# Optimization experiments

Hardware: AMD Instinct MI355X
Metric: run time of the kernel (lower is better)

Reference implementation:

```python
import jax, jax.numpy as jnp
import numpy as np

DIM = 192
HEADS = 6
WS = 8                      # window size (Wh = Ww = 8)
N = WS * WS                 # tokens per window = 64
NW = 1024                   # windows per image (256/8)^2
BATCH = 2
B_ = NW * BATCH             # 2048 windows total
TABLE = (2 * WS - 1) ** 2   # 225 relative-position entries


def _relative_position_index():
    coords = np.stack(np.meshgrid(np.arange(WS), np.arange(WS), indexing='ij'))  # (2,WS,WS)
    cf = coords.reshape(2, -1)                       # (2, N)
    rc = (cf[:, :, None] - cf[:, None, :]).transpose(1, 2, 0).astype(np.int64)  # (N,N,2)
    rc[..., 0] += WS - 1
    rc[..., 1] += WS - 1
    rc[..., 0] *= 2 * WS - 1
    return rc.sum(-1)                                # (N, N) in [0, TABLE)


def setup_inputs() -> dict:
    key = jax.random.key(0)
    ks = jax.random.split(key, 16)
    s = 0.02
    inp = {
        'x': jax.random.normal(ks[0], (B_, N, DIM), jnp.float32),
        'y': jax.random.normal(ks[1], (B_, N, DIM), jnp.float32),
        'mask_x': jnp.zeros((NW, N, N), jnp.float32),
        'mask_y': jnp.zeros((NW, N, N), jnp.float32),
        'qkv_w': jax.random.normal(ks[2], (3 * DIM, DIM), jnp.float32) * s,
        'qkv_b': jnp.zeros((3 * DIM,), jnp.float32),
        'kv_w': jax.random.normal(ks[3], (2 * DIM, DIM), jnp.float32) * s,
        'kv_b': jnp.zeros((2 * DIM,), jnp.float32),
        'rpb_x': jax.random.normal(ks[4], (TABLE, HEADS), jnp.float32) * s,
        'rpb_y': jax.random.normal(ks[5], (TABLE, HEADS), jnp.float32) * s,
        'merge1_w': jax.random.normal(ks[6], (DIM, 2 * DIM), jnp.float32) * s,
        'merge1_b': jnp.zeros((DIM,), jnp.float32),
        'merge2_w': jax.random.normal(ks[7], (DIM, DIM), jnp.float32) * s,
        'merge2_b': jnp.zeros((DIM,), jnp.float32),
        'proj_w': jax.random.normal(ks[8], (DIM, DIM), jnp.float32) * s,
        'proj_b': jnp.zeros((DIM,), jnp.float32),
        'rel_idx': jnp.asarray(_relative_position_index(), jnp.int32),
    }
    return inp


def _attend(q, k, v, table, rel_idx, mask):
    # q,k,v: (B_, H, N, hd); table: (TABLE, H); mask: (nW, N, N)
    b_, h, n, hd = q.shape
    bias = table[rel_idx].transpose(2, 0, 1)                 # (H, N, N)
    attn = jnp.einsum('bhnd,bhmd->bhnm', q, k) + bias[None]  # (B_, H, N, N)
    nW = mask.shape[0]
    attn = attn.reshape(b_ // nW, nW, h, n, n) + mask[None, :, None]
    attn = jax.nn.softmax(attn.reshape(b_, h, n, n), axis=-1)
    out = jnp.einsum('bhnm,bhmd->bhnd', attn, v)             # (B_, H, N, hd)
    return out.transpose(0, 2, 1, 3).reshape(b_, n, h * hd)


def reference(x, y, mask_x, mask_y, qkv_w, qkv_b, kv_w, kv_b, rpb_x, rpb_y,
              merge1_w, merge1_b, merge2_w, merge2_b, proj_w, proj_b, rel_idx):
    b_, n, c = x.shape
    hd = c // HEADS
    scale = hd ** (-0.5)
    qkv = (x @ qkv_w.T + qkv_b).reshape(b_, n, 3, HEADS, hd).transpose(2, 0, 3, 1, 4)
    q, k, v = qkv[0] * scale, qkv[1], qkv[2]
    x_self = _attend(q, k, v, rpb_x, rel_idx, mask_x)
    kv = (y @ kv_w.T + kv_b).reshape(b_, n, 2, HEADS, hd).transpose(2, 0, 3, 1, 4)
    x_cross = _attend(q, kv[0], kv[1], rpb_y, rel_idx, mask_y)
    m = jnp.concatenate([x_self, x_cross], axis=-1) @ merge1_w.T + merge1_b
    m = jax.nn.leaky_relu(m, negative_slope=0.2)
    m = m @ merge2_w.T + merge2_b
    return m @ proj_w.T + proj_b
```

## Files before the change

### kernel.cpp

```cpp
#include <hip/hip_runtime.h>

#define DEVINL __device__ __forceinline__

typedef __attribute__((ext_vector_type(8))) short          s16x8;
typedef __attribute__((ext_vector_type(8))) unsigned short u16x8;
typedef __attribute__((ext_vector_type(4))) unsigned short u16x4;
typedef __attribute__((ext_vector_type(4))) float          f32x4;

DEVINL unsigned short f2b(float f) {
    union { float f; unsigned int u; } c; c.f = f;
    return (unsigned short)((c.u + 0x7FFFu + ((c.u >> 16) & 1u)) >> 16);
}
DEVINL f32x4 mfma16(s16x8 a, s16x8 b, f32x4 c) {
    return __builtin_amdgcn_mfma_f32_16x16x32_bf16(a, b, c, 0, 0, 0);
}

#define QKV_ELEMS 110592
#define KV_ELEMS  73728
#define M1_ELEMS  73728
#define M2_ELEMS  36864
#define PW_ELEMS  36864
#define O_QKV 0
#define O_KV  110592
#define O_M1  184320
#define O_M2  258048
#define O_PW  294912
#define WB_ELEMS 331776
#define WB_BYTES (WB_ELEMS * 2)

#define LD_IN  200
#define LD_K   200
#define LD_VT  72
#define LD_P   72
#define LD_CAT 392
#define LD_M   200
#define OFF_R1 0
#define OFF_R2 12800
#define OFF_R3 25600
#define SMEM_ELEMS 39424
#define CATB OFF_R2

#define SCALE 0.17677669529663687f
#define LOG2E 1.4426950408889634f

__global__ __launch_bounds__(256) void cvt_w(
    const float* __restrict__ a, const float* __restrict__ b, const float* __restrict__ c,
    const float* __restrict__ d, const float* __restrict__ e, unsigned short* __restrict__ o)
{
    int i = (blockIdx.x * 256 + threadIdx.x) * 4;
    if (i >= WB_ELEMS) return;
    const float* s; int off;
    if (i < O_KV)      { s = a; off = i - O_QKV; }
    else if (i < O_M1) { s = b; off = i - O_KV; }
    else if (i < O_M2) { s = c; off = i - O_M1; }
    else if (i < O_PW) { s = d; off = i - O_M2; }
    else               { s = e; off = i - O_PW; }
    float4 v = *(const float4*)(s + off);
    u16x4 r;
    r[0] = f2b(v.x); r[1] = f2b(v.y); r[2] = f2b(v.z); r[3] = f2b(v.w);
    *(u16x4*)(o + i) = r;
}

template<bool WB>
DEVINL s16x8 loadB(const unsigned short* wbp, const float* wfp, int off) {
    if constexpr (WB) {
        return *(const s16x8*)(wbp + off);
    } else {
        float4 v0 = *(const float4*)(wfp + off);
        float4 v1 = *(const float4*)(wfp + off + 4);
        s16x8 r;
        r[0] = (short)f2b(v0.x); r[1] = (short)f2b(v0.y); r[2] = (short)f2b(v0.z); r[3] = (short)f2b(v0.w);
        r[4] = (short)f2b(v1.x); r[5] = (short)f2b(v1.y); r[6] = (short)f2b(v1.z); r[7] = (short)f2b(v1.w);
        return r;
    }
}

template<bool WB>
__global__ __launch_bounds__(512, 4) void swin_fused(
    const float* __restrict__ x,
    const float* __restrict__ y,
    const float* __restrict__ mask_x,
    const float* __restrict__ mask_y,
    const float* __restrict__ qkv_w,
    const float* __restrict__ qkv_b,
    const float* __restrict__ kv_w,
    const float* __restrict__ kv_b,
    const float* __restrict__ rpb_x,
    const float* __restrict__ rpb_y,
    const float* __restrict__ m1w,
    const float* __restrict__ m1b,
    const float* __restrict__ m2w,
    const float* __restrict__ m2b,
    const float* __restrict__ pw,
    const float* __restrict__ pb,
    const int* __restrict__ rel_idx,
    const unsigned short* __restrict__ wb,
    float* __restrict__ out)
{
    __shared__ __align__(16) unsigned short smem[SMEM_ELEMS];

    const int tid  = threadIdx.x;
    const int w    = tid >> 6;
    const int lane = tid & 63;
    const int l16  = lane & 15;
    const int quad = lane >> 4;
    const int wm   = w >> 2;
    const int wn   = w & 3;
    const int rb   = w >> 1;
    const int hh   = w & 1;
    const int b    = blockIdx.x;
    const int widx = b & 1023;

    const unsigned short* wqkv = WB ? wb + O_QKV : nullptr;
    const unsigned short* wkv  = WB ? wb + O_KV  : nullptr;
    const unsigned short* wm1  = WB ? wb + O_M1  : nullptr;
    const unsigned short* wm2  = WB ? wb + O_M2  : nullptr;
    const unsigned short* wpw  = WB ? wb + O_PW  : nullptr;

    {
        const float4* gx = (const float4*)(x + (size_t)b * 64 * 192);
        #pragma unroll
        for (int it = 0; it < 3; ++it) {
            int c = it * 512 + tid;
            int e = c * 8;
            int row = e / 192, col = e - row * 192;
            float4 v0 = gx[c * 2], v1 = gx[c * 2 + 1];
            u16x8 r;
            r[0] = f2b(v0.x); r[1] = f2b(v0.y); r[2] = f2b(v0.z); r[3] = f2b(v0.w);
            r[4] = f2b(v1.x); r[5] = f2b(v1.y); r[6] = f2b(v1.z); r[7] = f2b(v1.w);
            *(u16x8*)&smem[OFF_R1 + row * LD_IN + col] = r;
        }
    }
    __syncthreads();

    {
        s16x8 afr[2][6];
        #pragma unroll
        for (int mt = 0; mt < 2; ++mt)
            #pragma unroll
            for (int ks = 0; ks < 6; ++ks)
                afr[mt][ks] = *(const s16x8*)&smem[OFF_R1 + (wm * 32 + mt * 16 + l16) * LD_IN + ks * 32 + quad * 8];
        __syncthreads();

        #pragma unroll
        for (int nt = 0; nt < 9; ++nt) {
            int n0  = wn * 144 + nt * 16;
            int col = n0 + l16;
            f32x4 acc0 = {0,0,0,0}, acc1 = {0,0,0,0};
            #pragma unroll
            for (int ks = 0; ks < 6; ++ks) {
                s16x8 bf = loadB<WB>(wqkv, qkv_w, col * 192 + ks * 32 + quad * 8);
                acc0 = mfma16(afr[0][ks], bf, acc0);
                acc1 = mfma16(afr[1][ks], bf, acc1);
            }
            f32x4 accv[2] = {acc0, acc1};
            float bias = qkv_b[col];
            if (n0 < 192) {
                #pragma unroll
                for (int mt = 0; mt < 2; ++mt)
                    #pragma unroll
                    for (int r = 0; r < 4; ++r)
                        smem[OFF_R1 + (wm * 32 + mt * 16 + quad * 4 + r) * LD_K + col] =
                            f2b((accv[mt][r] + bias) * SCALE);
            } else if (n0 < 384) {
                #pragma unroll
                for (int mt = 0; mt < 2; ++mt)
                    #pragma unroll
                    for (int r = 0; r < 4; ++r)
                        smem[OFF_R2 + (wm * 32 + mt * 16 + quad * 4 + r) * LD_K + (col - 192)] =
                            f2b(accv[mt][r] + bias);
            } else {
                #pragma unroll
                for (int mt = 0; mt < 2; ++mt)
                    #pragma unroll
                    for (int r = 0; r < 4; ++r)
                        smem[OFF_R3 + (col - 384) * LD_VT + (wm * 32 + mt * 16 + quad * 4 + r)] =
                            f2b(accv[mt][r] + bias);
            }
        }
    }
    __syncthreads();

    s16x8 aQ[3];
    #pragma unroll
    for (int hl = 0; hl < 3; ++hl)
        aQ[hl] = *(const s16x8*)&smem[OFF_R1 + (rb * 16 + l16) * LD_K + (hh * 3 + hl) * 32 + quad * 8];
    __syncthreads();

    auto do_attn = [&](const float* __restrict__ rpb,
                       const float* __restrict__ mask,
                       unsigned (&opk)[12]) {
        unsigned idxp[8];
        #pragma unroll
        for (int p = 0; p < 8; ++p) {
            int ntt = p >> 1, r0 = (p & 1) * 2;
            int row = rb * 16 + quad * 4;
            int col = ntt * 16 + l16;
            unsigned lo = (unsigned)rel_idx[(row + r0)     * 64 + col] * 6u;
            unsigned hi = (unsigned)rel_idx[(row + r0 + 1) * 64 + col] * 6u;
            idxp[p] = lo | (hi << 16);
        }
        const float* mrow = mask + (size_t)widx * 4096 + (rb * 16 + quad * 4) * 64 + l16;
        const int pbase = OFF_R1 + w * 16 * LD_P;
        #pragma unroll
        for (int hl = 0; hl < 3; ++hl) {
            int h = hh * 3 + hl;
            f32x4 sacc[4];
            #pragma unroll
            for (int ntt = 0; ntt < 4; ++ntt) {
                s16x8 bK = *(const s16x8*)&smem[OFF_R2 + (ntt * 16 + l16) * LD_K + h * 32 + quad * 8];
                f32x4 z = {0,0,0,0};
                sacc[ntt] = mfma16(aQ[hl], bK, z);
            }
            float sv[4][4];
            #pragma unroll
            for (int ntt = 0; ntt < 4; ++ntt)
                #pragma unroll
                for (int r = 0; r < 4; ++r) {
                    unsigned idx6 = (idxp[ntt * 2 + (r >> 1)] >> ((r & 1) * 16)) & 0xFFFFu;
                    sv[ntt][r] = sacc[ntt][r] + rpb[idx6 + h] + mrow[r * 64 + ntt * 16];
                }
            float pv[4][4];
            #pragma unroll
            for (int r = 0; r < 4; ++r) {
                float mx = fmaxf(fmaxf(sv[0][r], sv[1][r]), fmaxf(sv[2][r], sv[3][r]));
                mx = fmaxf(mx, __shfl_xor(mx, 1));
                mx = fmaxf(mx, __shfl_xor(mx, 2));
                mx = fmaxf(mx, __shfl_xor(mx, 4));
                mx = fmaxf(mx, __shfl_xor(mx, 8));
                float e0 = __builtin_amdgcn_exp2f((sv[0][r] - mx) * LOG2E);
                float e1 = __builtin_amdgcn_exp2f((sv[1][r] - mx) * LOG2E);
                float e2 = __builtin_amdgcn_exp2f((sv[2][r] - mx) * LOG2E);
                float e3 = __builtin_amdgcn_exp2f((sv[3][r] - mx) * LOG2E);
                float s = e0 + e1 + e2 + e3;
                s += __shfl_xor(s, 1);
                s += __shfl_xor(s, 2);
                s += __shfl_xor(s, 4);
                s += __shfl_xor(s, 8);
                float inv = __builtin_amdgcn_rcpf(s);
                pv[0][r] = e0 * inv; pv[1][r] = e1 * inv; pv[2][r] = e2 * inv; pv[3][r] = e3 * inv;
            }
            #pragma unroll
            for (int ntt = 0; ntt < 4; ++ntt)
                #pragma unroll
                for (int r = 0; r < 4; ++r)
                    smem[pbase + (quad * 4 + r) * LD_P + ntt * 16 + l16] = f2b(pv[ntt][r]);
            f32x4 oh0 = {0,0,0,0}, oh1 = {0,0,0,0};
            #pragma unroll
            for (int kt = 0; kt < 2; ++kt) {
                s16x8 aP  = *(const s16x8*)&smem[pbase + l16 * LD_P + kt * 32 + quad * 8];
                s16x8 bV0 = *(const s16x8*)&smem[OFF_R3 + (h * 32 + l16) * LD_VT + kt * 32 + quad * 8];
                s16x8 bV1 = *(const s16x8*)&smem[OFF_R3 + (h * 32 + 16 + l16) * LD_VT + kt * 32 + quad * 8];
                oh0 = mfma16(aP, bV0, oh0);
                oh1 = mfma16(aP, bV1, oh1);
            }
            #pragma unroll
            for (int r = 0; r < 4; ++r)
                opk[hl * 4 + r] = (unsigned)f2b(oh0[r]) | ((unsigned)f2b(oh1[r]) << 16);
        }
    };

    unsigned opks[12];
    do_attn(rpb_x, mask_x, opks);
    __syncthreads();

    {
        const float4* gy = (const float4*)(y + (size_t)b * 64 * 192);
        #pragma unroll
        for (int it = 0; it < 3; ++it) {
            int c = it * 512 + tid;
            int e = c * 8;
            int row = e / 192, col = e - row * 192;
            float4 v0 = gy[c * 2], v1 = gy[c * 2 + 1];
            u16x8 r;
            r[0] = f2b(v0.x); r[1] = f2b(v0.y); r[2] = f2b(v0.z); r[3] = f2b(v0.w);
            r[4] = f2b(v1.x); r[5] = f2b(v1.y); r[6] = f2b(v1.z); r[7] = f2b(v1.w);
            *(u16x8*)&smem[OFF_R1 + row * LD_IN + col] = r;
        }
    }
    __syncthreads();

    {
        s16x8 afr[2][6];
        #pragma unroll
        for (int mt = 0; mt < 2; ++mt)
            #pragma unroll
            for (int ks = 0; ks < 6; ++ks)
                afr[mt][ks] = *(const s16x8*)&smem[OFF_R1 + (wm * 32 + mt * 16 + l16) * LD_IN + ks * 32 + quad * 8];

        #pragma unroll
        for (int nt = 0; nt < 6; ++nt) {
            int n0  = wn * 96 + nt * 16;
            int col = n0 + l16;
            f32x4 acc0 = {0,0,0,0}, acc1 = {0,0,0,0};
            #pragma unroll
            for (int ks = 0; ks < 6; ++ks) {
                s16x8 bf = loadB<WB>(wkv, kv_w, col * 192 + ks * 32 + quad * 8);
                acc0 = mfma16(afr[0][ks], bf, acc0);
                acc1 = mfma16(afr[1][ks], bf, acc1);
            }
            f32x4 accv[2] = {acc0, acc1};
            float bias = kv_b[col];
            if (n0 < 192) {
                #pragma unroll
                for (int mt = 0; mt < 2; ++mt)
                    #pragma unroll
                    for (int r = 0; r < 4; ++r)
                        smem[OFF_R2 + (wm * 32 + mt * 16 + quad * 4 + r) * LD_K + col] =
                            f2b(accv[mt][r] + bias);
            } else {
                #pragma unroll
                for (int mt = 0; mt < 2; ++mt)
                    #pragma unroll
                    for (int r = 0; r < 4; ++r)
                        smem[OFF_R3 + (col - 192) * LD_VT + (wm * 32 + mt * 16 + quad * 4 + r)] =
                            f2b(accv[mt][r] + bias);
            }
        }
    }
    __syncthreads();

    unsigned opkc[12];
    do_attn(rpb_y, mask_y, opkc);
    __syncthreads();

    #pragma unroll
    for (int hl = 0; hl < 3; ++hl) {
        int h = hh * 3 + hl;
        #pragma unroll
        for (int r = 0; r < 4; ++r) {
            int row = rb * 16 + quad * 4 + r;
            unsigned ps = opks[hl * 4 + r];
            unsigned pc = opkc[hl * 4 + r];
            smem[CATB + row * LD_CAT + h * 32 + l16]             = (unsigned short)(ps & 0xFFFFu);
            smem[CATB + row * LD_CAT + h * 32 + 16 + l16]        = (unsigned short)(ps >> 16);
            smem[CATB + row * LD_CAT + 192 + h * 32 + l16]       = (unsigned short)(pc & 0xFFFFu);
            smem[CATB + row * LD_CAT + 192 + h * 32 + 16 + l16]  = (unsigned short)(pc >> 16);
        }
    }
    __syncthreads();

    {
        f32x4 acc[3][2];
        #pragma unroll
        for (int nt = 0; nt < 3; ++nt) { f32x4 z = {0,0,0,0}; acc[nt][0] = z; acc[nt][1] = z; }
        #pragma unroll
        for (int ks = 0; ks < 12; ++ks) {
            s16x8 c0 = *(const s16x8*)&smem[CATB + (wm * 32 + l16) * LD_CAT + ks * 32 + quad * 8];
            s16x8 c1 = *(const s16x8*)&smem[CATB + (wm * 32 + 16 + l16) * LD_CAT + ks * 32 + quad * 8];
            #pragma unroll
            for (int nt = 0; nt < 3; ++nt) {
                int col = wn * 48 + nt * 16 + l16;
                s16x8 bf = loadB<WB>(wm1, m1w, col * 384 + ks * 32 + quad * 8);
                acc[nt][0] = mfma16(c0, bf, acc[nt][0]);
                acc[nt][1] = mfma16(c1, bf, acc[nt][1]);
            }
        }
        #pragma unroll
        for (int nt = 0; nt < 3; ++nt) {
            int col = wn * 48 + nt * 16 + l16;
            float bias = m1b[col];
            #pragma unroll
            for (int mt = 0; mt < 2; ++mt)
                #pragma unroll
                for (int r = 0; r < 4; ++r) {
                    float v = acc[nt][mt][r] + bias;
                    v = (v > 0.f) ? v : 0.2f * v;
                    smem[OFF_R1 + (wm * 32 + mt * 16 + quad * 4 + r) * LD_M + col] = f2b(v);
                }
        }
    }
    __syncthreads();

    {
        s16x8 afr[2][6];
        #pragma unroll
        for (int mt = 0; mt < 2; ++mt)
            #pragma unroll
            for (int ks = 0; ks < 6; ++ks)
                afr[mt][ks] = *(const s16x8*)&smem[OFF_R1 + (wm * 32 + mt * 16 + l16) * LD_M + ks * 32 + quad * 8];

        #pragma unroll
        for (int nt = 0; nt < 3; ++nt) {
            int n0  = wn * 48 + nt * 16;
            int col = n0 + l16;
            f32x4 acc0 = {0,0,0,0}, acc1 = {0,0,0,0};
            #pragma unroll
            for (int ks = 0; ks < 6; ++ks) {
                s16x8 bf = loadB<WB>(wm2, m2w, col * 192 + ks * 32 + quad * 8);
                acc0 = mfma16(afr[0][ks], bf, acc0);
                acc1 = mfma16(afr[1][ks], bf, acc1);
            }
            f32x4 accv[2] = {acc0, acc1};
            float bias = m2b[col];
            #pragma unroll
            for (int mt = 0; mt < 2; ++mt)
                #pragma unroll
                for (int r = 0; r < 4; ++r)
                    smem[OFF_R2 + (wm * 32 + mt * 16 + quad * 4 + r) * LD_M + col] = f2b(accv[mt][r] + bias);
        }
    }
    __syncthreads();

    {
        s16x8 afr[2][6];
        #pragma unroll
        for (int mt = 0; mt < 2; ++mt)
            #pragma unroll
            for (int ks = 0; ks < 6; ++ks)
                afr[mt][ks] = *(const s16x8*)&smem[OFF_R2 + (wm * 32 + mt * 16 + l16) * LD_M + ks * 32 + quad * 8];

        #pragma unroll
        for (int nt = 0; nt < 3; ++nt) {
            int n0  = wn * 48 + nt * 16;
            int col = n0 + l16;
            f32x4 acc0 = {0,0,0,0}, acc1 = {0,0,0,0};
            #pragma unroll
            for (int ks = 0; ks < 6; ++ks) {
                s16x8 bf = loadB<WB>(wpw, pw, col * 192 + ks * 32 + quad * 8);
                acc0 = mfma16(afr[0][ks], bf, acc0);
                acc1 = mfma16(afr[1][ks], bf, acc1);
            }
            f32x4 accv[2] = {acc0, acc1};
            float bias = pb[col];
            #pragma unroll
            for (int mt = 0; mt < 2; ++mt)
                #pragma unroll
                for (int r = 0; r < 4; ++r) {
                    int row = wm * 32 + mt * 16 + quad * 4 + r;
                    out[((size_t)b * 64 + row) * 192 + col] = accv[mt][r] + bias;
                }
        }
    }
}

extern "C" void kernel_launch(void* const* d_in, const int* in_sizes, int n_in,
                              void* d_out, int out_size, void* d_ws, size_t ws_size,
                              hipStream_t stream) {
    (void)in_sizes; (void)n_in; (void)out_size;
    const float* x    = (const float*)d_in[0];
    const float* y    = (const float*)d_in[1];
    const float* mx   = (const float*)d_in[2];
    const float* my   = (const float*)d_in[3];
    const float* qw   = (const float*)d_in[4];
    const float* qb   = (const float*)d_in[5];
    const float* kw   = (const float*)d_in[6];
    const float* kb   = (const float*)d_in[7];
    const float* rx   = (const float*)d_in[8];
    const float* ry   = (const float*)d_in[9];
    const float* m1w  = (const float*)d_in[10];
    const float* m1b  = (const float*)d_in[11];
    const float* m2w  = (const float*)d_in[12];
    const float* m2b  = (const float*)d_in[13];
    const float* pw   = (const float*)d_in[14];
    const float* pb   = (const float*)d_in[15];
    const int*   ridx = (const int*)d_in[16];
    float* out = (float*)d_out;

    if (ws_size >= (size_t)WB_BYTES) {
        unsigned short* wbuf = (unsigned short*)d_ws;
        cvt_w<<<WB_ELEMS / 4 / 256, 256, 0, stream>>>(qw, kw, m1w, m2w, pw, wbuf);
        swin_fused<true><<<2048, 512, 0, stream>>>(
            x, y, mx, my, qw, qb, kw, kb, rx, ry, m1w, m1b, m2w, m2b, pw, pb, ridx,
            wbuf, out);
    } else {
        swin_fused<false><<<2048, 512, 0, stream>>>(
            x, y, mx, my, qw, qb, kw, kb, rx, ry, m1w, m1b, m2w, m2b, pw, pb, ridx,
            nullptr, out);
    }
}
```

Measured before the change: 652.3 us.

## Process two windows per block to double weight reuse per B-fragment load

Each block now handles two 64-token windows (128 rows), so every weight fragment loaded from global memory feeds four MFMA row tiles instead of two. The grid halves to 1024 blocks, shared memory roughly doubles to about 154KB, and each warp does full six-head attention for one row block of one window. The aim is to halve weight traffic per token. The cost is more registers (launch bounds drop to two blocks per CU), lower occupancy, and fewer blocks to spread across CUs.

Result: faster. 523.9 us (-19.7%).

```diff
diff --git a/kernel.cpp b/kernel.cpp
--- a/kernel.cpp
+++ b/kernel.cpp
@@ -35,9 +35,10 @@
 #define LD_CAT 392
 #define LD_M   200
 #define OFF_R1 0
-#define OFF_R2 12800
-#define OFF_R3 25600
-#define SMEM_ELEMS 39424
+#define OFF_R2 25600
+#define OFF_R3 51200
+#define VT_WIN 13824
+#define SMEM_ELEMS 78848
 #define CATB OFF_R2
 
 #define SCALE 0.17677669529663687f
@@ -76,7 +77,7 @@
 }
 
 template<bool WB>
-__global__ __launch_bounds__(512, 4) void swin_fused(
+__global__ __launch_bounds__(512, 2) void swin_fused(
     const float* __restrict__ x,
     const float* __restrict__ y,
     const float* __restrict__ mask_x,
@@ -104,12 +105,11 @@
     const int lane = tid & 63;
     const int l16  = lane & 15;
     const int quad = lane >> 4;
+    const int wn   = w & 3;
     const int wm   = w >> 2;
-    const int wn   = w & 3;
-    const int rb   = w >> 1;
-    const int hh   = w & 1;
+    const int win  = w >> 2;
+    const int rb   = w & 3;
     const int b    = blockIdx.x;
-    const int widx = b & 1023;
 
     const unsigned short* wqkv = WB ? wb + O_QKV : nullptr;
     const unsigned short* wkv  = WB ? wb + O_KV  : nullptr;
@@ -118,9 +118,9 @@
     const unsigned short* wpw  = WB ? wb + O_PW  : nullptr;
 
     {
-        const float4* gx = (const float4*)(x + (size_t)b * 64 * 192);
-        #pragma unroll
-        for (int it = 0; it < 3; ++it) {
+        const float4* gx = (const float4*)(x + (size_t)b * 128 * 192);
+        #pragma unroll
+        for (int it = 0; it < 6; ++it) {
             int c = it * 512 + tid;
             int e = c * 8;
             int row = e / 192, col = e - row * 192;
@@ -134,62 +134,65 @@
     __syncthreads();
 
     {
-        s16x8 afr[2][6];
-        #pragma unroll
-        for (int mt = 0; mt < 2; ++mt)
+        s16x8 afr[4][6];
+        #pragma unroll
+        for (int mt = 0; mt < 4; ++mt)
             #pragma unroll
             for (int ks = 0; ks < 6; ++ks)
-                afr[mt][ks] = *(const s16x8*)&smem[OFF_R1 + (wm * 32 + mt * 16 + l16) * LD_IN + ks * 32 + quad * 8];
+                afr[mt][ks] = *(const s16x8*)&smem[OFF_R1 + (wm * 64 + mt * 16 + l16) * LD_IN + ks * 32 + quad * 8];
         __syncthreads();
 
         #pragma unroll
         for (int nt = 0; nt < 9; ++nt) {
             int n0  = wn * 144 + nt * 16;
             int col = n0 + l16;
-            f32x4 acc0 = {0,0,0,0}, acc1 = {0,0,0,0};
+            f32x4 a0 = {0,0,0,0}, a1 = {0,0,0,0}, a2 = {0,0,0,0}, a3 = {0,0,0,0};
             #pragma unroll
             for (int ks = 0; ks < 6; ++ks) {
                 s16x8 bf = loadB<WB>(wqkv, qkv_w, col * 192 + ks * 32 + quad * 8);
-                acc0 = mfma16(afr[0][ks], bf, acc0);
-                acc1 = mfma16(afr[1][ks], bf, acc1);
-            }
-            f32x4 accv[2] = {acc0, acc1};
+                a0 = mfma16(afr[0][ks], bf, a0);
+                a1 = mfma16(afr[1][ks], bf, a1);
+                a2 = mfma16(afr[2][ks], bf, a2);
+                a3 = mfma16(afr[3][ks], bf, a3);
+            }
+            f32x4 accv[4] = {a0, a1, a2, a3};
             float bias = qkv_b[col];
             if (n0 < 192) {
                 #pragma unroll
-                for (int mt = 0; mt < 2; ++mt)
+                for (int mt = 0; mt < 4; ++mt)
                     #pragma unroll
                     for (int r = 0; r < 4; ++r)
-                        smem[OFF_R1 + (wm * 32 + mt * 16 + quad * 4 + r) * LD_K + col] =
+                        smem[OFF_R1 + (wm * 64 + mt * 16 + quad * 4 + r) * LD_K + col] =
                             f2b((accv[mt][r] + bias) * SCALE);
             } else if (n0 < 384) {
                 #pragma unroll
-                for (int mt = 0; mt < 2; ++mt)
+                for (int mt = 0; mt < 4; ++mt)
                     #pragma unroll
                     for (int r = 0; r < 4; ++r)
-                        smem[OFF_R2 + (wm * 32 + mt * 16 + quad * 4 + r) * LD_K + (col - 192)] =
+                        smem[OFF_R2 + (wm * 64 + mt * 16 + quad * 4 + r) * LD_K + (col - 192)] =
                             f2b(accv[mt][r] + bias);
             } else {
                 #pragma unroll
-                for (int mt = 0; mt < 2; ++mt)
+                for (int mt = 0; mt < 4; ++mt)
                     #pragma unroll
                     for (int r = 0; r < 4; ++r)
-                        smem[OFF_R3 + (col - 384) * LD_VT + (wm * 32 + mt * 16 + quad * 4 + r)] =
+                        smem[OFF_R3 + wm * VT_WIN + (col - 384) * LD_VT + (mt * 16 + quad * 4 + r)] =
                             f2b(accv[mt][r] + bias);
             }
         }
     }
     __syncthreads();
 
-    s16x8 aQ[3];
+    s16x8 aQ[6];
     #pragma unroll
-    for (int hl = 0; hl < 3; ++hl)
-        aQ[hl] = *(const s16x8*)&smem[OFF_R1 + (rb * 16 + l16) * LD_K + (hh * 3 + hl) * 32 + quad * 8];
+    for (int h = 0; h < 6; ++h)
+        aQ[h] = *(const s16x8*)&smem[OFF_R1 + (win * 64 + rb * 16 + l16) * LD_K + h * 32 + quad * 8];
     __syncthreads();
 
     auto do_attn = [&](const float* __restrict__ rpb,
                        const float* __restrict__ mask,
-                       unsigned (&opk)[12]) {
+                       unsigned (&opk)[24]) {
+        int widx = (b * 2 + win) & 1023;
         unsigned idxp[8];
         #pragma unroll
         for (int p = 0; p < 8; ++p) {
@@ -203,14 +206,13 @@
         const float* mrow = mask + (size_t)widx * 4096 + (rb * 16 + quad * 4) * 64 + l16;
         const int pbase = OFF_R1 + w * 16 * LD_P;
         #pragma unroll
-        for (int hl = 0; hl < 3; ++hl) {
-            int h = hh * 3 + hl;
+        for (int h = 0; h < 6; ++h) {
             f32x4 sacc[4];
             #pragma unroll
             for (int ntt = 0; ntt < 4; ++ntt) {
-                s16x8 bK = *(const s16x8*)&smem[OFF_R2 + (ntt * 16 + l16) * LD_K + h * 32 + quad * 8];
+                s16x8 bK = *(const s16x8*)&smem[OFF_R2 + (win * 64 + ntt * 16 + l16) * LD_K + h * 32 + quad * 8];
                 f32x4 z = {0,0,0,0};
-                sacc[ntt] = mfma16(aQ[hl], bK, z);
+                sacc[ntt] = mfma16(aQ[h], bK, z);
             }
             float sv[4][4];
             #pragma unroll
@@ -249,25 +251,25 @@
             #pragma unroll
             for (int kt = 0; kt < 2; ++kt) {
                 s16x8 aP  = *(const s16x8*)&smem[pbase + l16 * LD_P + kt * 32 + quad * 8];
-                s16x8 bV0 = *(const s16x8*)&smem[OFF_R3 + (h * 32 + l16) * LD_VT + kt * 32 + quad * 8];
-                s16x8 bV1 = *(const s16x8*)&smem[OFF_R3 + (h * 32 + 16 + l16) * LD_VT + kt * 32 + quad * 8];
+                s16x8 bV0 = *(const s16x8*)&smem[OFF_R3 + win * VT_WIN + (h * 32 + l16) * LD_VT + kt * 32 + quad * 8];
+                s16x8 bV1 = *(const s16x8*)&smem[OFF_R3 + win * VT_WIN + (h * 32 + 16 + l16) * LD_VT + kt * 32 + quad * 8];
                 oh0 = mfma16(aP, bV0, oh0);
                 oh1 = mfma16(aP, bV1, oh1);
             }
             #pragma unroll
             for (int r = 0; r < 4; ++r)
-                opk[hl * 4 + r] = (unsigned)f2b(oh0[r]) | ((unsigned)f2b(oh1[r]) << 16);
+                opk[h * 4 + r] = (unsigned)f2b(oh0[r]) | ((unsigned)f2b(oh1[r]) << 16);
         }
     };
 
-    unsigned opks[12];
+    unsigned opks[24];
     do_attn(rpb_x, mask_x, opks);
     __syncthreads();
 
     {
-        const float4* gy = (const float4*)(y + (size_t)b * 64 * 192);
-        #pragma unroll
-        for (int it = 0; it < 3; ++it) {
+        const float4* gy = (const float4*)(y + (size_t)b * 128 * 192);
+        #pragma unroll
+        for (int it = 0; it < 6; ++it) {
             int c = it * 512 + tid;
             int e = c * 8;
             int row = e / 192, col = e - row * 192;
@@ -281,57 +283,58 @@
     __syncthreads();
 
     {
-        s16x8 afr[2][6];
-        #pragma unroll
-        for (int mt = 0; mt < 2; ++mt)
+        s16x8 afr[4][6];
+        #pragma unroll
+        for (int mt = 0; mt < 4; ++mt)
             #pragma unroll
             for (int ks = 0; ks < 6; ++ks)
-                afr[mt][ks] = *(const s16x8*)&smem[OFF_R1 + (wm * 32 + mt * 16 + l16) * LD_IN + ks * 32 + quad * 8];
+                afr[mt][ks] = *(const s16x8*)&smem[OFF_R1 + (wm * 64 + mt * 16 + l16) * LD_IN + ks * 32 + quad * 8];
 
         #pragma unroll
         for (int nt = 0; nt < 6; ++nt) {
             int n0  = wn * 96 + nt * 16;
             int col = n0 + l16;
-            f32x4 acc0 = {0,0,0,0}, acc1 = {0,0,0,0};
+            f32x4 a0 = {0,0,0,0}, a1 = {0,0,0,0}, a2 = {0,0,0,0}, a3 = {0,0,0,0};
             #pragma unroll
             for (int ks = 0; ks < 6; ++ks) {
                 s16x8 bf = loadB<WB>(wkv, kv_w, col * 192 + ks * 32 + quad * 8);
-                acc0 = mfma16(afr[0][ks], bf, acc0);
-                acc1 = mfma16(afr[1][ks], bf, acc1);
-            }
-            f32x4 accv[2] = {acc0, acc1};
+                a0 = mfma16(afr[0][ks], bf, a0);
+                a1 = mfma16(afr[1][ks], bf, a1);
+                a2 = mfma16(afr[2][ks], bf, a2);
+                a3 = mfma16(afr[3][ks], bf, a3);
+            }
+            f32x4 accv[4] = {a0, a1, a2, a3};
             float bias = kv_b[col];
             if (n0 < 192) {
                 #pragma unroll
-                for (int mt = 0; mt < 2; ++mt)
+                for (int mt = 0; mt < 4; ++mt)
                     #pragma unroll
                     for (int r = 0; r < 4; ++r)
-                        smem[OFF_R2 + (wm * 32 + mt * 16 + quad * 4 + r) * LD_K + col] =
+                        smem[OFF_R2 + (wm * 64 + mt * 16 + quad * 4 + r) * LD_K + col] =
                             f2b(accv[mt][r] + bias);
             } else {
                 #pragma unroll
-                for (int mt = 0; mt < 2; ++mt)
+                for (int mt = 0; mt < 4; ++mt)
                     #pragma unroll
                     for (int r = 0; r < 4; ++r)
-                        smem[OFF_R3 + (col - 192) * LD_VT + (wm * 32 + mt * 16 + quad * 4 + r)] =
+                        smem[OFF_R3 + wm * VT_WIN + (col - 192) * LD_VT + (mt * 16 + quad * 4 + r)] =
                             f2b(accv[mt][r] + bias);
             }
         }
     }
     __syncthreads();
 
-    unsigned opkc[12];
+    unsigned opkc[24];
     do_attn(rpb_y, mask_y, opkc);
     __syncthreads();
 
     #pragma unroll
-    for (int hl = 0; hl < 3; ++hl) {
-        int h = hh * 3 + hl;
+    for (int h = 0; h < 6; ++h) {
         #pragma unroll
         for (int r = 0; r < 4; ++r) {
-            int row = rb * 16 + quad * 4 + r;
-            unsigned ps = opks[hl * 4 + r];
-            unsigned pc = opkc[hl * 4 + r];
+            int row = win * 64 + rb * 16 + quad * 4 + r;
+            unsigned ps = opks[h * 4 + r];
+            unsigned pc = opkc[h * 4 + r];
             smem[CATB + row * LD_CAT + h * 32 + l16]             = (unsigned short)(ps & 0xFFFFu);
             smem[CATB + row * LD_CAT + h * 32 + 16 + l16]        = (unsigned short)(ps >> 16);
             smem[CATB + row * LD_CAT + 192 + h * 32 + l16]       = (unsigned short)(pc & 0xFFFFu);
@@ -341,19 +344,24 @@
     __syncthreads();
 
     {
-        f32x4 acc[3][2];
-        #pragma unroll
-        for (int nt = 0; nt < 3; ++nt) { f32x4 z = {0,0,0,0}; acc[nt][0] = z; acc[nt][1] = z; }
+        f32x4 acc[3][4];
+        #pragma unroll
+        for (int nt = 0; nt < 3; ++nt)
+            #pragma unroll
+            for (int mt = 0; mt < 4; ++mt) { f32x4 z = {0,0,0,0}; acc[nt][mt] = z; }
         #pragma unroll
         for (int ks = 0; ks < 12; ++ks) {
-            s16x8 c0 = *(const s16x8*)&smem[CATB + (wm * 32 + l16) * LD_CAT + ks * 32 + quad * 8];
-            s16x8 c1 = *(const s16x8*)&smem[CATB + (wm * 32 + 16 + l16) * LD_CAT + ks * 32 + quad * 8];
+            s16x8 cm[4];
+            #pragma unroll
+            for (int mt = 0; mt < 4; ++mt)
+                cm[mt] = *(const s16x8*)&smem[CATB + (wm * 64 + mt * 16 + l16) * LD_CAT + ks * 32 + quad * 8];
             #pragma unroll
             for (int nt = 0; nt < 3; ++nt) {
                 int col = wn * 48 + nt * 16 + l16;
                 s16x8 bf = loadB<WB>(wm1, m1w, col * 384 + ks * 32 + quad * 8);
-                acc[nt][0] = mfma16(c0, bf, acc[nt][0]);
-                acc[nt][1] = mfma16(c1, bf, acc[nt][1]);
+                #pragma unroll
+                for (int mt = 0; mt < 4; ++mt)
+                    acc[nt][mt] = mfma16(cm[mt], bf, acc[nt][mt]);
             }
         }
         #pragma unroll
@@ -361,74 +369,76 @@
             int col = wn * 48 + nt * 16 + l16;
             float bias = m1b[col];
             #pragma unroll
-            for (int mt = 0; mt < 2; ++mt)
+            for (int mt = 0; mt < 4; ++mt)
                 #pragma unroll
                 for (int r = 0; r < 4; ++r) {
                     float v = acc[nt][mt][r] + bias;
                     v = (v > 0.f) ? v : 0.2f * v;
-                    smem[OFF_R1 + (wm * 32 + mt * 16 + quad * 4 + r) * LD_M + col] = f2b(v);
+                    smem[OFF_R1 + (wm * 64 + mt * 16 + quad * 4 + r) * LD_M + col] = f2b(v);
                 }
         }
     }
     __syncthreads();
 
     {
-        s16x8 afr[2][6];
-        #pragma unroll
-        for (int mt = 0; mt < 2; ++mt)
+        s16x8 afr[4][6];
+        #pragma unroll
+        for (int mt = 0; mt < 4; ++mt)
             #pragma unroll
             for (int ks = 0; ks < 6; ++ks)
-                afr[mt][ks] = *(const s16x8*)&smem[OFF_R1 + (wm * 32 + mt * 16 + l16) * LD_M + ks * 32 + quad * 8];
+                afr[mt][ks] = *(const s16x8*)&smem[OFF_R1 + (wm * 64 + mt * 16 + l16) * LD_M + ks * 32 + quad * 8];
 
         #pragma unroll
         for (int nt = 0; nt < 3; ++nt) {
-            int n0  = wn * 48 + nt * 16;
-            int col = n0 + l16;
-            f32x4 acc0 = {0,0,0,0}, acc1 = {0,0,0,0};
+            int col = wn * 48 + nt * 16 + l16;
+            f32x4 a0 = {0,0,0,0}, a1 = {0,0,0,0}, a2 = {0,0,0,0}, a3 = {0,0,0,0};
             #pragma unroll
             for (int ks = 0; ks < 6; ++ks) {
                 s16x8 bf = loadB<WB>(wm2, m2w, col * 192 + ks * 32 + quad * 8);
-                acc0 = mfma16(afr[0][ks], bf, acc0);
-                acc1 = mfma16(afr[1][ks], bf, acc1);
-            }
-            f32x4 accv[2] = {acc0, acc1};
+                a0 = mfma16(afr[0][ks], bf, a0);
+                a1 = mfma16(afr[1][ks], bf, a1);
+                a2 = mfma16(afr[2][ks], bf, a2);
+                a3 = mfma16(afr[3][ks], bf, a3);
+            }
+            f32x4 accv[4] = {a0, a1, a2, a3};
             float bias = m2b[col];
             #pragma unroll
-            for (int mt = 0; mt < 2; ++mt)
+            for (int mt = 0; mt < 4; ++mt)
                 #pragma unroll
                 for (int r = 0; r < 4; ++r)
-                    smem[OFF_R2 + (wm * 32 + mt * 16 + quad * 4 + r) * LD_M + col] = f2b(accv[mt][r] + bias);
-        }
-    }
-    __syncthreads();
-
-    {
-        s16x8 afr[2][6];
-        #pragma unroll
-        for (int mt = 0; mt < 2; ++mt)
+                    smem[OFF_R2 + (wm * 64 + mt * 16 + quad * 4 + r) * LD_M + col] = f2b(accv[mt][r] + bias);
+        }
+    }
+    __syncthreads();
+
+    {
+        s16x8 afr[4][6];
+        #pragma unroll
+        for (int mt = 0; mt < 4; ++mt)
             #pragma unroll
             for (int ks = 0; ks < 6; ++ks)
-                afr[mt][ks] = *(const s16x8*)&smem[OFF_R2 + (wm * 32 + mt * 16 + l16) * LD_M + ks * 32 + quad * 8];
+                afr[mt][ks] = *(const s16x8*)&smem[OFF_R2 + (wm * 64 + mt * 16 + l16) * LD_M + ks * 32 + quad * 8];
 
         #pragma unroll
         for (int nt = 0; nt < 3; ++nt) {
-            int n0  = wn * 48 + nt * 16;
-            int col = n0 + l16;
-            f32x4 acc0 = {0,0,0,0}, acc1 = {0,0,0,0};
+            int col = wn * 48 + nt * 16 + l16;
+            f32x4 a0 = {0,0,0,0}, a1 = {0,0,0,0}, a2 = {0,0,0,0}, a3 = {0,0,0,0};
             #pragma unroll
             for (int ks = 0; ks < 6; ++ks) {
                 s16x8 bf = loadB<WB>(wpw, pw, col * 192 + ks * 32 + quad * 8);
-                acc0 = mfma16(afr[0][ks], bf, acc0);
-                acc1 = mfma16(afr[1][ks], bf, acc1);
-            }
-            f32x4 accv[2] = {acc0, acc1};
+                a0 = mfma16(afr[0][ks], bf, a0);
+                a1 = mfma16(afr[1][ks], bf, a1);
+                a2 = mfma16(afr[2][ks], bf, a2);
+                a3 = mfma16(afr[3][ks], bf, a3);
+            }
+            f32x4 accv[4] = {a0, a1, a2, a3};
             float bias = pb[col];
             #pragma unroll
-            for (int mt = 0; mt < 2; ++mt)
+            for (int mt = 0; mt < 4; ++mt)
                 #pragma unroll
                 for (int r = 0; r < 4; ++r) {
-                    int row = wm * 32 + mt * 16 + quad * 4 + r;
-                    out[((size_t)b * 64 + row) * 192 + col] = accv[mt][r] + bias;
+                    int row = wm * 64 + mt * 16 + quad * 4 + r;
+                    out[((size_t)b * 128 + row) * 192 + col] = accv[mt][r] + bias;
                 }
         }
     }
@@ -460,11 +470,11 @@
     if (ws_size >= (size_t)WB_BYTES) {
         unsigned short* wbuf = (unsigned short*)d_ws;
         cvt_w<<<WB_ELEMS / 4 / 256, 256, 0, stream>>>(qw, kw, m1w, m2w, pw, wbuf);
-        swin_fused<true><<<2048, 512, 0, stream>>>(
+        swin_fused<true><<<1024, 512, 0, stream>>>(
             x, y, mx, my, qw, qb, kw, kb, rx, ry, m1w, m1b, m2w, m2b, pw, pb, ridx,
             wbuf, out);
     } else {
-        swin_fused<false><<<2048, 512, 0, stream>>>(
+        swin_fused<false><<<1024, 512, 0, stream>>>(
             x, y, mx, my, qw, qb, kw, kb, rx, ry, m1w, m1b, m2w, m2b, pw, pb, ridx,
             nullptr, out);
     }
```

## Process two windows per block with 1024 threads and doubled shared memory

Applied to the files above, without the earlier changes.

Each block now handles two attention windows (128 tokens) with 16 waves instead of one window with 8 waves. The grid is halved and shared-memory regions are doubled, with a per-window V-transpose buffer. Each wave in the projection GEMMs now covers its existing 32-row M tile across a 128-row tile, so every weight fragment loaded from global memory feeds more MFMA work. The cost is about 154 KB of LDS per block, which probably limits each CU to one block, plus heavier barrier synchronisation across 16 waves.

Result: slower. 699.7 us (+7.3%).

```diff
diff --git a/kernel.cpp b/kernel.cpp
--- a/kernel.cpp
+++ b/kernel.cpp
@@ -35,9 +35,10 @@
 #define LD_CAT 392
 #define LD_M   200
 #define OFF_R1 0
-#define OFF_R2 12800
-#define OFF_R3 25600
-#define SMEM_ELEMS 39424
+#define OFF_R2 25600
+#define OFF_R3 51200
+#define VT_WIN 13824
+#define SMEM_ELEMS 78848
 #define CATB OFF_R2
 
 #define SCALE 0.17677669529663687f
@@ -76,7 +77,7 @@
 }
 
 template<bool WB>
-__global__ __launch_bounds__(512, 4) void swin_fused(
+__global__ __launch_bounds__(1024, 4) void swin_fused(
     const float* __restrict__ x,
     const float* __restrict__ y,
     const float* __restrict__ mask_x,
@@ -104,12 +105,12 @@
     const int lane = tid & 63;
     const int l16  = lane & 15;
     const int quad = lane >> 4;
+    const int wn   = w & 3;
     const int wm   = w >> 2;
-    const int wn   = w & 3;
-    const int rb   = w >> 1;
+    const int win  = w >> 3;
+    const int rb   = (w >> 1) & 3;
     const int hh   = w & 1;
     const int b    = blockIdx.x;
-    const int widx = b & 1023;
 
     const unsigned short* wqkv = WB ? wb + O_QKV : nullptr;
     const unsigned short* wkv  = WB ? wb + O_KV  : nullptr;
@@ -118,10 +119,10 @@
     const unsigned short* wpw  = WB ? wb + O_PW  : nullptr;
 
     {
-        const float4* gx = (const float4*)(x + (size_t)b * 64 * 192);
+        const float4* gx = (const float4*)(x + (size_t)b * 128 * 192);
         #pragma unroll
         for (int it = 0; it < 3; ++it) {
-            int c = it * 512 + tid;
+            int c = it * 1024 + tid;
             int e = c * 8;
             int row = e / 192, col = e - row * 192;
             float4 v0 = gx[c * 2], v1 = gx[c * 2 + 1];
@@ -146,14 +147,14 @@
         for (int nt = 0; nt < 9; ++nt) {
             int n0  = wn * 144 + nt * 16;
             int col = n0 + l16;
-            f32x4 acc0 = {0,0,0,0}, acc1 = {0,0,0,0};
+            f32x4 a0 = {0,0,0,0}, a1 = {0,0,0,0};
             #pragma unroll
             for (int ks = 0; ks < 6; ++ks) {
                 s16x8 bf = loadB<WB>(wqkv, qkv_w, col * 192 + ks * 32 + quad * 8);
-                acc0 = mfma16(afr[0][ks], bf, acc0);
-                acc1 = mfma16(afr[1][ks], bf, acc1);
-            }
-            f32x4 accv[2] = {acc0, acc1};
+                a0 = mfma16(afr[0][ks], bf, a0);
+                a1 = mfma16(afr[1][ks], bf, a1);
+            }
+            f32x4 accv[2] = {a0, a1};
             float bias = qkv_b[col];
             if (n0 < 192) {
                 #pragma unroll
@@ -173,9 +174,11 @@
                 #pragma unroll
                 for (int mt = 0; mt < 2; ++mt)
                     #pragma unroll
-                    for (int r = 0; r < 4; ++r)
-                        smem[OFF_R3 + (col - 384) * LD_VT + (wm * 32 + mt * 16 + quad * 4 + r)] =
+                    for (int r = 0; r < 4; ++r) {
+                        int tok = (wm & 1) * 32 + mt * 16 + quad * 4 + r;
+                        smem[OFF_R3 + (wm >> 1) * VT_WIN + (col - 384) * LD_VT + tok] =
                             f2b(accv[mt][r] + bias);
+                    }
             }
         }
     }
@@ -184,12 +187,13 @@
     s16x8 aQ[3];
     #pragma unroll
     for (int hl = 0; hl < 3; ++hl)
-        aQ[hl] = *(const s16x8*)&smem[OFF_R1 + (rb * 16 + l16) * LD_K + (hh * 3 + hl) * 32 + quad * 8];
+        aQ[hl] = *(const s16x8*)&smem[OFF_R1 + (win * 64 + rb * 16 + l16) * LD_K + (hh * 3 + hl) * 32 + quad * 8];
     __syncthreads();
 
     auto do_attn = [&](const float* __restrict__ rpb,
                        const float* __restrict__ mask,
                        unsigned (&opk)[12]) {
+        int widx = (b * 2 + win) & 1023;
         unsigned idxp[8];
         #pragma unroll
         for (int p = 0; p < 8; ++p) {
@@ -208,7 +212,7 @@
             f32x4 sacc[4];
             #pragma unroll
             for (int ntt = 0; ntt < 4; ++ntt) {
-                s16x8 bK = *(const s16x8*)&smem[OFF_R2 + (ntt * 16 + l16) * LD_K + h * 32 + quad * 8];
+                s16x8 bK = *(const s16x8*)&smem[OFF_R2 + (win * 64 + ntt * 16 + l16) * LD_K + h * 32 + quad * 8];
                 f32x4 z = {0,0,0,0};
                 sacc[ntt] = mfma16(aQ[hl], bK, z);
             }
@@ -249,8 +253,8 @@
             #pragma unroll
             for (int kt = 0; kt < 2; ++kt) {
                 s16x8 aP  = *(const s16x8*)&smem[pbase + l16 * LD_P + kt * 32 + quad * 8];
-                s16x8 bV0 = *(const s16x8*)&smem[OFF_R3 + (h * 32 + l16) * LD_VT + kt * 32 + quad * 8];
-                s16x8 bV1 = *(const s16x8*)&smem[OFF_R3 + (h * 32 + 16 + l16) * LD_VT + kt * 32 + quad * 8];
+                s16x8 bV0 = *(const s16x8*)&smem[OFF_R3 + win * VT_WIN + (h * 32 + l16) * LD_VT + kt * 32 + quad * 8];
+                s16x8 bV1 = *(const s16x8*)&smem[OFF_R3 + win * VT_WIN + (h * 32 + 16 + l16) * LD_VT + kt * 32 + quad * 8];
                 oh0 = mfma16(aP, bV0, oh0);
                 oh1 = mfma16(aP, bV1, oh1);
             }
@@ -265,10 +269,10 @@
     __syncthreads();
 
     {
-        const float4* gy = (const float4*)(y + (size_t)b * 64 * 192);
+        const float4* gy = (const float4*)(y + (size_t)b * 128 * 192);
         #pragma unroll
         for (int it = 0; it < 3; ++it) {
-            int c = it * 512 + tid;
+            int c = it * 1024 + tid;
             int e = c * 8;
             int row = e / 192, col = e - row * 192;
             float4 v0 = gy[c * 2], v1 = gy[c * 2 + 1];
@@ -292,14 +296,14 @@
         for (int nt = 0; nt < 6; ++nt) {
             int n0  = wn * 96 + nt * 16;
             int col = n0 + l16;
-            f32x4 acc0 = {0,0,0,0}, acc1 = {0,0,0,0};
+            f32x4 a0 = {0,0,0,0}, a1 = {0,0,0,0};
             #pragma unroll
             for (int ks = 0; ks < 6; ++ks) {
                 s16x8 bf = loadB<WB>(wkv, kv_w, col * 192 + ks * 32 + quad * 8);
-                acc0 = mfma16(afr[0][ks], bf, acc0);
-                acc1 = mfma16(afr[1][ks], bf, acc1);
-            }
-            f32x4 accv[2] = {acc0, acc1};
+                a0 = mfma16(afr[0][ks], bf, a0);
+                a1 = mfma16(afr[1][ks], bf, a1);
+            }
+            f32x4 accv[2] = {a0, a1};
             float bias = kv_b[col];
             if (n0 < 192) {
                 #pragma unroll
@@ -312,9 +316,11 @@
                 #pragma unroll
                 for (int mt = 0; mt < 2; ++mt)
                     #pragma unroll
-                    for (int r = 0; r < 4; ++r)
-                        smem[OFF_R3 + (col - 192) * LD_VT + (wm * 32 + mt * 16 + quad * 4 + r)] =
+                    for (int r = 0; r < 4; ++r) {
+                        int tok = (wm & 1) * 32 + mt * 16 + quad * 4 + r;
+                        smem[OFF_R3 + (wm >> 1) * VT_WIN + (col - 192) * LD_VT + tok] =
                             f2b(accv[mt][r] + bias);
+                    }
             }
         }
     }
@@ -329,7 +335,7 @@
         int h = hh * 3 + hl;
         #pragma unroll
         for (int r = 0; r < 4; ++r) {
-            int row = rb * 16 + quad * 4 + r;
+            int row = win * 64 + rb * 16 + quad * 4 + r;
             unsigned ps = opks[hl * 4 + r];
             unsigned pc = opkc[hl * 4 + r];
             smem[CATB + row * LD_CAT + h * 32 + l16]             = (unsigned short)(ps & 0xFFFFu);
@@ -382,16 +388,15 @@
 
         #pragma unroll
         for (int nt = 0; nt < 3; ++nt) {
-            int n0  = wn * 48 + nt * 16;
-            int col = n0 + l16;
-            f32x4 acc0 = {0,0,0,0}, acc1 = {0,0,0,0};
+            int col = wn * 48 + nt * 16 + l16;
+            f32x4 a0 = {0,0,0,0}, a1 = {0,0,0,0};
             #pragma unroll
             for (int ks = 0; ks < 6; ++ks) {
                 s16x8 bf = loadB<WB>(wm2, m2w, col * 192 + ks * 32 + quad * 8);
-                acc0 = mfma16(afr[0][ks], bf, acc0);
-                acc1 = mfma16(afr[1][ks], bf, acc1);
-            }
-            f32x4 accv[2] = {acc0, acc1};
+                a0 = mfma16(afr[0][ks], bf, a0);
+                a1 = mfma16(afr[1][ks], bf, a1);
+            }
+            f32x4 accv[2] = {a0, a1};
             float bias = m2b[col];
             #pragma unroll
             for (int mt = 0; mt < 2; ++mt)
@@ -412,23 +417,22 @@
 
         #pragma unroll
         for (int nt = 0; nt < 3; ++nt) {
-            int n0  = wn * 48 + nt * 16;
-            int col = n0 + l16;
-            f32x4 acc0 = {0,0,0,0}, acc1 = {0,0,0,0};
+            int col = wn * 48 + nt * 16 + l16;
+            f32x4 a0 = {0,0,0,0}, a1 = {0,0,0,0};
             #pragma unroll
             for (int ks = 0; ks < 6; ++ks) {
                 s16x8 bf = loadB<WB>(wpw, pw, col * 192 + ks * 32 + quad * 8);
-                acc0 = mfma16(afr[0][ks], bf, acc0);
-                acc1 = mfma16(afr[1][ks], bf, acc1);
-            }
-            f32x4 accv[2] = {acc0, acc1};
+                a0 = mfma16(afr[0][ks], bf, a0);
+                a1 = mfma16(afr[1][ks], bf, a1);
+            }
+            f32x4 accv[2] = {a0, a1};
             float bias = pb[col];
             #pragma unroll
             for (int mt = 0; mt < 2; ++mt)
                 #pragma unroll
                 for (int r = 0; r < 4; ++r) {
                     int row = wm * 32 + mt * 16 + quad * 4 + r;
-                    out[((size_t)b * 64 + row) * 192 + col] = accv[mt][r] + bias;
+                    out[((size_t)b * 128 + row) * 192 + col] = accv[mt][r] + bias;
                 }
         }
     }
@@ -460,11 +464,11 @@
     if (ws_size >= (size_t)WB_BYTES) {
         unsigned short* wbuf = (unsigned short*)d_ws;
         cvt_w<<<WB_ELEMS / 4 / 256, 256, 0, stream>>>(qw, kw, m1w, m2w, pw, wbuf);
-        swin_fused<true><<<2048, 512, 0, stream>>>(
+        swin_fused<true><<<1024, 1024, 0, stream>>>(
             x, y, mx, my, qw, qb, kw, kb, rx, ry, m1w, m1b, m2w, m2b, pw, pb, ridx,
             wbuf, out);
     } else {
-        swin_fused<false><<<2048, 512, 0, stream>>>(
+        swin_fused<false><<<1024, 1024, 0, stream>>>(
             x, y, mx, my, qw, qb, kw, kb, rx, ry, m1w, m1b, m2w, m2b, pw, pb, ridx,
             nullptr, out);
     }
```
